# Performance work log

Measured on AMD Instinct MI355X. Metric: run time of the kernel, lower is better.

Reference implementation:

```python
import jax, jax.numpy as jnp
import numpy as np

B, S, H, R = 32, 1024, 768, 24
ATT_EPS = 1e10
LN_EPS = 1e-12


def setup_inputs() -> dict:
    key = jax.random.key(0)
    ks = jax.random.split(key, 20)
    sc = 0.02
    inp = {
        "relation": jax.random.randint(ks[0], (B, 1), 0, R),
        "last_hidden_size": jax.random.normal(ks[1], (B, S, H), dtype=jnp.float32),
        "sub_head": jax.random.randint(ks[2], (B, 1), 0, S),
        "sub_tail": jax.random.randint(ks[3], (B, 1), 0, S),
        "attention_mask": jnp.ones((B, S), dtype=jnp.float32),
        # learned parameters
        "rel_emb": jax.random.normal(ks[4], (R, H)) * sc,
        "W_rf": jax.random.normal(ks[5], (H, H)) * sc,
        "b_rf": jnp.zeros((H,), jnp.float32),
        "gamma": jnp.ones((H,), jnp.float32),
        "beta": jnp.zeros((H,), jnp.float32),
        "W_wd": jax.random.normal(ks[6], (H, 2 * H)) * sc,
        "W_bd": jax.random.normal(ks[7], (H, 2 * H)) * sc,
        "Wq": jax.random.normal(ks[8], (H, H)) * sc,
        "bq": jnp.zeros((H,), jnp.float32),
        "Wk": jax.random.normal(ks[9], (H, H)) * sc,
        "bk": jnp.zeros((H,), jnp.float32),
        "Wv": jax.random.normal(ks[10], (H, H)) * sc,
        "bv": jnp.zeros((H,), jnp.float32),
        "W_obj": jax.random.normal(ks[11], (1, H)) * sc,
        "b_obj": jnp.zeros((1,), jnp.float32),
    }
    return inp


def reference(relation, last_hidden_size, sub_head, sub_tail, attention_mask,
              rel_emb, W_rf, b_rf, gamma, beta, W_wd, W_bd,
              Wq, bq, Wk, bk, Wv, bv, W_obj, b_obj):
    # dropout layers are identity in eval mode
    # relation feature: embedding -> linear -> ReLU6   [B,1,H]
    rel_feature = jnp.clip(rel_emb[relation] @ W_rf.T + b_rf, 0.0, 6.0)
    # subject span features via gather                 [B,1,H]
    sh = jnp.take_along_axis(last_hidden_size, sub_head[:, :, None], axis=1)
    st = jnp.take_along_axis(last_hidden_size, sub_tail[:, :, None], axis=1)
    sub_feature = (sh + st) * 0.5
    cond = jnp.concatenate([rel_feature, sub_feature], axis=-1)  # [B,1,2H]

    # conditional layer norm: per-sample affine from condition
    weight = cond @ W_wd.T + gamma  # [B,1,H]
    bias = cond @ W_bd.T + beta     # [B,1,H]
    mean = jnp.mean(last_hidden_size, axis=-1, keepdims=True)
    ctr = last_hidden_size - mean
    var = jnp.mean(ctr * ctr, axis=-1, keepdims=True)
    x = ctr / jnp.sqrt(var + LN_EPS)
    x = x * weight + bias  # [B,S,H]

    # custom attention: ReLU-activated q/k/v, additive mask bias, residual
    q = jax.nn.relu(x @ Wq.T + bq)
    k = jax.nn.relu(x @ Wk.T + bk)
    v = jax.nn.relu(x @ Wv.T + bv)
    e = jnp.einsum('bsh,bth->bst', q, k)  # [B,S,S]
    e = e - ATT_EPS * (1.0 - attention_mask[:, None, :])
    a = jax.nn.softmax(e, axis=-1)
    hidden = jnp.einsum('bst,bth->bsh', a, v) + x  # residual

    pred_obj_head = jnp.squeeze(hidden @ W_obj.T + b_obj, axis=-1)  # [B,S]
    return pred_obj_head, hidden
```

## Files before the change

kernel.cpp:

```cpp
#include <hip/hip_runtime.h>

constexpr int NB  = 32;
constexpr int NS  = 1024;
constexpr int NH  = 768;
constexpr int NH2 = 1536;
constexpr int NQKV = 2304;
constexpr int NBS = NB * NS;

typedef __bf16 bf16x8 __attribute__((ext_vector_type(8)));
typedef float  f32x4  __attribute__((ext_vector_type(4)));
typedef unsigned short u16x8 __attribute__((ext_vector_type(8)));

__device__ __forceinline__ unsigned short f2bf(float f) {
  unsigned int u = __builtin_bit_cast(unsigned int, f);
  u += 0x7FFFu + ((u >> 16) & 1u);
  return (unsigned short)(u >> 16);
}
__device__ __forceinline__ float bf2f(unsigned short h) {
  return __builtin_bit_cast(float, ((unsigned int)h) << 16);
}

#define GLDS16(g, l)                                                         \
  __builtin_amdgcn_global_load_lds(                                          \
      (__attribute__((address_space(1))) void*)(g),                          \
      (__attribute__((address_space(3))) void*)(l), 16, 0, 0)

#define SBAR()    asm volatile("s_barrier" ::: "memory")
#define WAITVM6() asm volatile("s_waitcnt vmcnt(6)" ::: "memory")
#define WAITVM0() asm volatile("s_waitcnt vmcnt(0)" ::: "memory")
#define LGKM0()                                                              \
  do {                                                                       \
    asm volatile("s_waitcnt lgkmcnt(0)" ::: "memory");                       \
    __builtin_amdgcn_sched_barrier(0);                                       \
  } while (0)

__launch_bounds__(256)
__global__ void cond_pre(const int* __restrict__ relation,
                         const float* __restrict__ h,
                         const int* __restrict__ subh,
                         const int* __restrict__ subt,
                         const float* __restrict__ rel_emb,
                         float* __restrict__ reT, float* __restrict__ condT) {
  const int b = blockIdx.x, t = threadIdx.x;
  const int r = relation[b], sh = subh[b], st = subt[b];
  for (int k = t; k < NH; k += 256) {
    reT[(size_t)k * NB + b] = rel_emb[(size_t)r * NH + k];
    condT[(size_t)(NH + k) * NB + b] =
        0.5f * (h[((size_t)b * NS + sh) * NH + k] +
                h[((size_t)b * NS + st) * NH + k]);
  }
}

__launch_bounds__(256)
__global__ void cond_rf(const float* __restrict__ W_rf,
                        const float* __restrict__ b_rf,
                        const float* __restrict__ reT,
                        float* __restrict__ condT) {
  const int t = threadIdx.x;
  const int b = t & 31, jl = t >> 5;
  const int j = blockIdx.x * 8 + jl;
  const float4* w4 = (const float4*)(W_rf + (size_t)j * NH);
  const float* rT = reT + b;
  float a0 = 0.f, a1 = 0.f;
  for (int k4 = 0; k4 < NH / 4; k4++) {
    float4 w = w4[k4];
    const float* c = rT + (size_t)(k4 * 4) * NB;
    a0 += w.x * c[0] + w.y * c[NB];
    a1 += w.z * c[2 * NB] + w.w * c[3 * NB];
  }
  float acc = a0 + a1 + b_rf[j];
  condT[(size_t)j * NB + b] = fminf(fmaxf(acc, 0.0f), 6.0f);
}

__launch_bounds__(256)
__global__ void cond_wb(const float* __restrict__ W_wd,
                        const float* __restrict__ W_bd,
                        const float* __restrict__ gamma,
                        const float* __restrict__ beta,
                        const float* __restrict__ condT,
                        float* __restrict__ wt, float* __restrict__ bs) {
  __shared__ float redW[128], redB[128];
  const int t = threadIdx.x;
  const int b = t & 31, jl = (t >> 5) & 3, ks = t >> 7;
  const int j = blockIdx.x * 4 + jl;
  const float4* ww = (const float4*)(W_wd + (size_t)j * NH2 + ks * NH);
  const float4* wb = (const float4*)(W_bd + (size_t)j * NH2 + ks * NH);
  const float* cT = condT + (size_t)ks * NH * NB + b;
  float aw0 = 0.f, aw1 = 0.f, ab0 = 0.f, ab1 = 0.f;
  for (int k4 = 0; k4 < NH / 4; k4++) {
    float4 w = ww[k4];
    float4 v = wb[k4];
    const float* c = cT + (size_t)(k4 * 4) * NB;
    float c0 = c[0], c1 = c[NB], c2 = c[2 * NB], c3 = c[3 * NB];
    aw0 += w.x * c0 + w.y * c1;
    aw1 += w.z * c2 + w.w * c3;
    ab0 += v.x * c0 + v.y * c1;
    ab1 += v.z * c2 + v.w * c3;
  }
  float aw = aw0 + aw1, ab = ab0 + ab1;
  if (ks == 1) {
    redW[t - 128] = aw;
    redB[t - 128] = ab;
  }
  __syncthreads();
  if (ks == 0) {
    aw += redW[t];
    ab += redB[t];
    wt[(size_t)b * NH + j] = aw + gamma[j];
    bs[(size_t)b * NH + j] = ab + beta[j];
  }
}

__launch_bounds__(64)
__global__ void ln_kernel(const float* __restrict__ h,
                          const float* __restrict__ wt,
                          const float* __restrict__ bs,
                          unsigned short* __restrict__ xbf) {
  const int row = blockIdx.x;
  const int b = row >> 10;
  const int lane = threadIdx.x;
  const float4* hr = (const float4*)(h + (size_t)row * NH);
  float4 v0 = hr[lane], v1 = hr[lane + 64], v2 = hr[lane + 128];
  float sum = 0.f, sq = 0.f;
  {
    sum += v0.x + v0.y + v0.z + v0.w;
    sq  += v0.x * v0.x + v0.y * v0.y + v0.z * v0.z + v0.w * v0.w;
    sum += v1.x + v1.y + v1.z + v1.w;
    sq  += v1.x * v1.x + v1.y * v1.y + v1.z * v1.z + v1.w * v1.w;
    sum += v2.x + v2.y + v2.z + v2.w;
    sq  += v2.x * v2.x + v2.y * v2.y + v2.z * v2.z + v2.w * v2.w;
  }
  for (int off = 32; off > 0; off >>= 1) {
    sum += __shfl_xor(sum, off, 64);
    sq  += __shfl_xor(sq, off, 64);
  }
  const float mean = sum * (1.0f / NH);
  const float var  = sq * (1.0f / NH) - mean * mean;
  const float rstd = rsqrtf(var + 1e-12f);
  const float4* wr = (const float4*)(wt + (size_t)b * NH);
  const float4* br = (const float4*)(bs + (size_t)b * NH);
  ushort4* xr = (ushort4*)(xbf + (size_t)row * NH);
#pragma unroll
  for (int i = 0; i < 3; i++) {
    float4 v = (i == 0) ? v0 : (i == 1) ? v1 : v2;
    float4 w = wr[lane + 64 * i];
    float4 bb = br[lane + 64 * i];
    ushort4 o;
    o.x = f2bf((v.x - mean) * rstd * w.x + bb.x);
    o.y = f2bf((v.y - mean) * rstd * w.y + bb.y);
    o.z = f2bf((v.z - mean) * rstd * w.z + bb.z);
    o.w = f2bf((v.w - mean) * rstd * w.w + bb.w);
    xr[lane + 64 * i] = o;
  }
}

__launch_bounds__(256)
__global__ void prep_w(const float* __restrict__ Wq, const float* __restrict__ bq,
                       const float* __restrict__ Wk, const float* __restrict__ bk,
                       const float* __restrict__ Wv, const float* __restrict__ bv,
                       unsigned short* __restrict__ Wcat, float* __restrict__ bcat) {
  const int row = blockIdx.x;
  const float* Wsrc;
  const float* bsrc;
  int r;
  if (row < NH) { Wsrc = Wq; bsrc = bq; r = row; }
  else if (row < NH2) { Wsrc = Wk; bsrc = bk; r = row - NH; }
  else { Wsrc = Wv; bsrc = bv; r = row - NH2; }
  for (int j = threadIdx.x; j < NH; j += 256)
    Wcat[(size_t)row * NH + j] = f2bf(Wsrc[(size_t)r * NH + j]);
  if (threadIdx.x == 0) bcat[row] = bsrc[r];
}

template <int OUT_BF16, int RELU, int HASBIAS, int RES>
__launch_bounds__(512, 2)
__global__ void gemm256(const unsigned short* __restrict__ A, long long sAz, int lda,
                        const unsigned short* __restrict__ Bm, long long sBz, int ldb,
                        void* __restrict__ C, long long sCz, int ldc,
                        const float* __restrict__ bias,
                        const unsigned short* __restrict__ Res, long long sRz, int ldr,
                        int K) {
  extern __shared__ char lds[];
  const int t = threadIdx.x;
  const int z = blockIdx.z;
  int id = blockIdx.x + blockIdx.y * gridDim.x;
  {
    const int nwg = gridDim.x * gridDim.y;
    const int q = nwg >> 3, r = nwg & 7;
    const int xcd = id & 7, lid = id >> 3;
    id = (xcd < r ? xcd * (q + 1) : r * (q + 1) + (xcd - r) * q) + lid;
  }
  const int tileN = (id % gridDim.x) * 256;
  const int tileM = (id / gridDim.x) * 256;
  const unsigned short* Ab = A + (size_t)z * sAz + (size_t)tileM * lda;
  const unsigned short* Bb = Bm + (size_t)z * sBz + (size_t)tileN * ldb;

  const int lane = t & 63;
  const int w = t >> 6;
  const int wm = w >> 2, wn = w & 3;
  const int lr = lane & 15, hi = lane >> 4;
  const int swz = (lr & 7) << 4;
  const int brow0 = (wn & 1) * 64;

  const int sr = t >> 3;
  const int scc = (t & 7) ^ (sr & 7);

#define STAGEH(Gb, ld, kc, dst)                                             \
  do {                                                                      \
    GLDS16((Gb) + (size_t)sr * (ld) + (kc) + scc * 8, (dst) + (size_t)t * 16); \
    GLDS16((Gb) + (size_t)(64 + sr) * (ld) + (kc) + scc * 8,                \
           (dst) + 8192 + (size_t)t * 16);                                  \
  } while (0)

#define RD_BALL(Bh)                                                         \
  do {                                                                      \
    _Pragma("unroll") for (int nn_ = 0; nn_ < 4; nn_++)                     \
      _Pragma("unroll") for (int ks_ = 0; ks_ < 2; ks_++)                   \
        bF[nn_][ks_] = *(const bf16x8*)((Bh) + (brow0 + nn_ * 16 + lr) * 128 + \
                                        ((ks_ * 64 + hi * 16) ^ swz));      \
  } while (0)

#define RD_AH(m0, Ah)                                                       \
  do {                                                                      \
    _Pragma("unroll") for (int mm_ = 0; mm_ < 4; mm_++)                     \
      _Pragma("unroll") for (int ks_ = 0; ks_ < 2; ks_++)                   \
        aF[mm_][ks_] = *(const bf16x8*)((Ah) + (((m0) + mm_) * 16 + lr) * 128 + \
                                        ((ks_ * 64 + hi * 16) ^ swz));      \
  } while (0)

#define MFMAQ(mb, nb)                                                       \
  do {                                                                      \
    __builtin_amdgcn_s_setprio(1);                                          \
    _Pragma("unroll") for (int ks_ = 0; ks_ < 2; ks_++)                     \
      _Pragma("unroll") for (int mm_ = 0; mm_ < 4; mm_++)                   \
        _Pragma("unroll") for (int nn_ = 0; nn_ < 2; nn_++)                 \
          acc[(mb) + mm_][(nb) + nn_] = __builtin_amdgcn_mfma_f32_16x16x32_bf16( \
              aF[mm_][ks_], bF[(nb) + nn_][ks_], acc[(mb) + mm_][(nb) + nn_], \
              0, 0, 0);                                                     \
    __builtin_amdgcn_s_setprio(0);                                          \
  } while (0)

  f32x4 acc[8][4];
#pragma unroll
  for (int m = 0; m < 8; m++)
#pragma unroll
    for (int n = 0; n < 4; n++) acc[m][n] = (f32x4)0.0f;

  const int NT = K >> 6;

  STAGEH(Bb, ldb, 0, lds + 65536);
  STAGEH(Bb + (size_t)128 * ldb, ldb, 0, lds + 65536 + 16384);
  STAGEH(Ab, lda, 0, lds);
  STAGEH(Ab + (size_t)128 * lda, lda, 0, lds + 16384);
  STAGEH(Bb, ldb, 64, lds + 65536 + 32768);
  STAGEH(Bb + (size_t)128 * ldb, ldb, 64, lds + 65536 + 32768 + 16384);
  STAGEH(Ab, lda, 64, lds + 32768);
  WAITVM6();
  SBAR();

  for (int kt = 0; kt < NT; kt++) {
    const int bc = kt & 1;
    const char* Ah = lds + bc * 32768 + wm * 16384;
    const char* Bh = lds + 65536 + bc * 32768 + (wn >> 1) * 16384;
    bf16x8 aF[4][2], bF[4][2];
    RD_BALL(Bh);
    RD_AH(0, Ah);
    if (kt + 1 < NT)
      STAGEH(Ab + (size_t)128 * lda, lda, (kt + 1) * 64,
             lds + (bc ^ 1) * 32768 + 16384);
    SBAR();
    LGKM0();
    MFMAQ(0, 0);
    SBAR();
    if (kt + 2 < NT)
      STAGEH(Bb, ldb, (kt + 2) * 64, lds + 65536 + bc * 32768);
    SBAR();
    MFMAQ(0, 2);
    SBAR();
    RD_AH(4, Ah);
    if (kt + 2 < NT)
      STAGEH(Bb + (size_t)128 * ldb, ldb, (kt + 2) * 64,
             lds + 65536 + bc * 32768 + 16384);
    SBAR();
    LGKM0();
    MFMAQ(4, 2);
    SBAR();
    if (kt + 2 < NT)
      STAGEH(Ab, lda, (kt + 2) * 64, lds + bc * 32768);
    SBAR();
    MFMAQ(4, 0);
    if (kt + 2 < NT) {
      WAITVM6();
    } else if (kt + 1 < NT) {
      WAITVM0();
    }
    SBAR();
  }

  const int row0 = tileM + wm * 128;
  const int col0 = tileN + wn * 64;
#pragma unroll
  for (int m = 0; m < 8; m++) {
    const int rowb = row0 + m * 16 + hi * 4;
#pragma unroll
    for (int n = 0; n < 4; n++) {
      const int col = col0 + n * 16 + lr;
      const float bv = HASBIAS ? bias[col] : 0.0f;
      f32x4 v = acc[m][n];
#pragma unroll
      for (int r = 0; r < 4; r++) {
        float x = v[r] + bv;
        if (RELU) x = fmaxf(x, 0.0f);
        if (RES)
          x += bf2f(Res[(size_t)z * sRz + (size_t)(rowb + r) * ldr + col]);
        if (OUT_BF16)
          ((unsigned short*)C)[(size_t)z * sCz + (size_t)(rowb + r) * ldc + col] =
              f2bf(x);
        else
          ((float*)C)[(size_t)z * sCz + (size_t)(rowb + r) * ldc + col] = x;
      }
    }
  }
#undef STAGEH
#undef RD_BALL
#undef RD_AH
#undef MFMAQ
}

__launch_bounds__(256)
__global__ void softmax_kernel(float* __restrict__ e,
                               const float* __restrict__ mask, int b0) {
  const int ri = blockIdx.x;
  const int lb = blockIdx.y;
  const int b = b0 + lb;
  float* row = e + ((size_t)lb * NS + ri) * NS;
  const int t = threadIdx.x;
  float4 v = ((const float4*)row)[t];
  float4 m = ((const float4*)(mask + (size_t)b * NS))[t];
  v.x -= 1e10f * (1.0f - m.x);
  v.y -= 1e10f * (1.0f - m.y);
  v.z -= 1e10f * (1.0f - m.z);
  v.w -= 1e10f * (1.0f - m.w);
  float mx = fmaxf(fmaxf(v.x, v.y), fmaxf(v.z, v.w));
  __shared__ float red[4];
  for (int off = 32; off > 0; off >>= 1) mx = fmaxf(mx, __shfl_xor(mx, off, 64));
  if ((t & 63) == 0) red[t >> 6] = mx;
  __syncthreads();
  mx = fmaxf(fmaxf(red[0], red[1]), fmaxf(red[2], red[3]));
  const float e0 = __expf(v.x - mx), e1 = __expf(v.y - mx);
  const float e2 = __expf(v.z - mx), e3 = __expf(v.w - mx);
  float sm = e0 + e1 + e2 + e3;
  __syncthreads();
  for (int off = 32; off > 0; off >>= 1) sm += __shfl_xor(sm, off, 64);
  if ((t & 63) == 0) red[t >> 6] = sm;
  __syncthreads();
  sm = red[0] + red[1] + red[2] + red[3];
  const float inv = 1.0f / sm;
  ushort4 o;
  o.x = f2bf(e0 * inv);
  o.y = f2bf(e1 * inv);
  o.z = f2bf(e2 * inv);
  o.w = f2bf(e3 * inv);
  ((ushort4*)row)[t] = o;
}

__launch_bounds__(256)
__global__ void transpose_v(const unsigned short* __restrict__ qkv,
                            unsigned short* __restrict__ vT) {
  const int b = blockIdx.z;
  const int s0 = blockIdx.x * 64;
  const int h0 = blockIdx.y * 64;
  __shared__ unsigned short tile[64][72];
  const int t = threadIdx.x;
  const int tx = t & 7, ty = t >> 3;
  const unsigned short* src = qkv + ((size_t)(b * NS + s0)) * NQKV + NH2 + h0;
#pragma unroll
  for (int i = 0; i < 2; i++) {
    const int s = ty + 32 * i;
    u16x8 vv = *(const u16x8*)(src + (size_t)s * NQKV + tx * 8);
#pragma unroll
    for (int j = 0; j < 8; j++) tile[s][tx * 8 + j] = vv[j];
  }
  __syncthreads();
  unsigned short* dst = vT + ((size_t)b * NH + h0) * NS + s0;
#pragma unroll
  for (int i = 0; i < 2; i++) {
    const int hh = ty + 32 * i;
    u16x8 o;
#pragma unroll
    for (int j = 0; j < 8; j++) o[j] = tile[tx * 8 + j][hh];
    *(u16x8*)(dst + (size_t)hh * NS + tx * 8) = o;
  }
}

__launch_bounds__(64)
__global__ void pred_kernel(const float* __restrict__ hidden,
                            const float* __restrict__ wobj,
                            const float* __restrict__ bobj,
                            float* __restrict__ pred) {
  const int row = blockIdx.x;
  const int lane = threadIdx.x;
  const float4* hr = (const float4*)(hidden + (size_t)row * NH);
  const float4* wr = (const float4*)wobj;
  float s = 0.f;
#pragma unroll
  for (int i = 0; i < 3; i++) {
    float4 a = hr[lane + 64 * i];
    float4 w = wr[lane + 64 * i];
    s += a.x * w.x + a.y * w.y + a.z * w.z + a.w * w.w;
  }
  for (int off = 32; off > 0; off >>= 1) s += __shfl_xor(s, off, 64);
  if (lane == 0) pred[row] = s + bobj[0];
}

extern "C" void kernel_launch(void* const* d_in, const int* in_sizes, int n_in,
                              void* d_out, int out_size, void* d_ws,
                              size_t ws_size, hipStream_t stream) {
  const int* relation   = (const int*)d_in[0];
  const float* lhs      = (const float*)d_in[1];
  const int* sub_head   = (const int*)d_in[2];
  const int* sub_tail   = (const int*)d_in[3];
  const float* att_mask = (const float*)d_in[4];
  const float* rel_emb  = (const float*)d_in[5];
  const float* W_rf     = (const float*)d_in[6];
  const float* b_rf     = (const float*)d_in[7];
  const float* gamma    = (const float*)d_in[8];
  const float* beta     = (const float*)d_in[9];
  const float* W_wd     = (const float*)d_in[10];
  const float* W_bd     = (const float*)d_in[11];
  const float* Wq       = (const float*)d_in[12];
  const float* bq       = (const float*)d_in[13];
  const float* Wk       = (const float*)d_in[14];
  const float* bk       = (const float*)d_in[15];
  const float* Wv       = (const float*)d_in[16];
  const float* bv       = (const float*)d_in[17];
  const float* W_obj    = (const float*)d_in[18];
  const float* b_obj    = (const float*)d_in[19];

  char* ws = (char*)d_ws;
  unsigned short* Wcat = (unsigned short*)(ws + 0);
  float* bcat  = (float*)(ws + 3538944);
  float* wt    = (float*)(ws + 3548160);
  float* bs    = (float*)(ws + 3646464);
  float* reT   = (float*)(ws + 3744768);
  float* condT = (float*)(ws + 3843072);
  unsigned short* xbf = (unsigned short*)(ws + 4039680);
  unsigned short* qkv = (unsigned short*)(ws + 54371328);
  unsigned short* vT  = (unsigned short*)(ws + 205366272);
  float* ebuf = (float*)(ws + 255697920);

  float* out_pred = (float*)d_out;
  float* out_hidden = out_pred + NBS;

  const size_t fixed = 255697920ull;
  size_t avail = ws_size > fixed ? ws_size - fixed : 0;
  int CB = 32;
  while (CB > 1 && (size_t)CB * (size_t)NS * NS * 4 > avail) CB >>= 1;

  prep_w<<<dim3(NQKV), dim3(256), 0, stream>>>(Wq, bq, Wk, bk, Wv, bv, Wcat, bcat);
  cond_pre<<<dim3(NB), dim3(256), 0, stream>>>(relation, lhs, sub_head, sub_tail,
                                               rel_emb, reT, condT);
  cond_rf<<<dim3(NH / 8), dim3(256), 0, stream>>>(W_rf, b_rf, reT, condT);
  cond_wb<<<dim3(NH / 4), dim3(256), 0, stream>>>(W_wd, W_bd, gamma, beta, condT,
                                                  wt, bs);
  ln_kernel<<<dim3(NBS), dim3(64), 0, stream>>>(lhs, wt, bs, xbf);

  gemm256<1, 1, 1, 0><<<dim3(NQKV / 256, NBS / 256, 1), dim3(512), 131072, stream>>>(
      xbf, 0, NH, Wcat, 0, NH, qkv, 0, NQKV, bcat, nullptr, 0, 0, NH);

  transpose_v<<<dim3(NS / 64, NH / 64, NB), dim3(256), 0, stream>>>(qkv, vT);

  for (int b0 = 0; b0 < NB; b0 += CB) {
    gemm256<0, 0, 0, 0><<<dim3(NS / 256, NS / 256, CB), dim3(512), 131072, stream>>>(
        qkv + (size_t)b0 * NS * NQKV, (long long)NS * NQKV, NQKV,
        qkv + (size_t)b0 * NS * NQKV + NH, (long long)NS * NQKV, NQKV,
        ebuf, (long long)NS * NS, NS, nullptr, nullptr, 0, 0, NH);
    softmax_kernel<<<dim3(NS, CB), dim3(256), 0, stream>>>(ebuf, att_mask, b0);
    gemm256<0, 0, 0, 1><<<dim3(NH / 256, NS / 256, CB), dim3(512), 131072, stream>>>(
        (const unsigned short*)ebuf, (long long)NS * 2048, 2048,
        vT + (size_t)b0 * NH * NS, (long long)NH * NS, NS,
        out_hidden + (size_t)b0 * NS * NH, (long long)NS * NH, NH, nullptr,
        xbf + (size_t)b0 * NS * NH, (long long)NS * NH, NH, NS);
  }

  pred_kernel<<<dim3(NBS), dim3(64), 0, stream>>>(out_hidden, W_obj, b_obj,
                                                  out_pred);
}
```

Measured before the change: 494.4 us.

## Fuse V transpose and prediction head into GEMM epilogues, split Q/K layout

The QKV GEMM epilogue now writes Q and K to separate contiguous buffers and writes V directly in transposed layout, which removes the transpose_v kernel. The final P·V GEMM epilogue computes the W_obj dot product per row with shuffles and atomically accumulates into a pred buffer that is zeroed beforehand, which removes the pred_kernel pass over hidden. Softmax now writes bf16 probabilities to a separate compact buffer instead of overwriting the fp32 scores in place. In exchange, the transposed V stores are strided and scattered, and the atomics make pred accumulation order nondeterministic.

```diff
diff --git a/kernel.cpp b/kernel.cpp
--- a/kernel.cpp
+++ b/kernel.cpp
@@ -171,14 +171,17 @@
   if (threadIdx.x == 0) bcat[row] = bsrc[r];
 }
 
-template <int OUT_BF16, int RELU, int HASBIAS, int RES>
+template <int OUT_BF16, int RELU, int HASBIAS, int RES, int SPLIT3, int FPRED>
 __launch_bounds__(512, 2)
 __global__ void gemm256(const unsigned short* __restrict__ A, long long sAz, int lda,
                         const unsigned short* __restrict__ Bm, long long sBz, int ldb,
                         void* __restrict__ C, long long sCz, int ldc,
                         const float* __restrict__ bias,
                         const unsigned short* __restrict__ Res, long long sRz, int ldr,
-                        int K) {
+                        int K, unsigned short* __restrict__ vTp,
+                        const float* __restrict__ wobj,
+                        const float* __restrict__ bobj,
+                        float* __restrict__ pred) {
   extern __shared__ char lds[];
   const int t = threadIdx.x;
   const int z = blockIdx.z;
@@ -301,6 +304,7 @@
 #pragma unroll
   for (int m = 0; m < 8; m++) {
     const int rowb = row0 + m * 16 + hi * 4;
+    float psum[4] = {0.f, 0.f, 0.f, 0.f};
 #pragma unroll
     for (int n = 0; n < 4; n++) {
       const int col = col0 + n * 16 + lr;
@@ -312,11 +316,37 @@
         if (RELU) x = fmaxf(x, 0.0f);
         if (RES)
           x += bf2f(Res[(size_t)z * sRz + (size_t)(rowb + r) * ldr + col]);
-        if (OUT_BF16)
+        if (SPLIT3) {
+          const int seg = col >= NH2 ? 2 : (col >= NH ? 1 : 0);
+          if (seg < 2) {
+            ((unsigned short*)C)[(size_t)seg * NBS * NH +
+                                 (size_t)(rowb + r) * NH + (col - seg * NH)] =
+                f2bf(x);
+          } else {
+            vTp[((size_t)((rowb + r) >> 10) * NH + (col - NH2)) * NS +
+                ((rowb + r) & (NS - 1))] = f2bf(x);
+          }
+        } else if (OUT_BF16) {
           ((unsigned short*)C)[(size_t)z * sCz + (size_t)(rowb + r) * ldc + col] =
               f2bf(x);
-        else
+        } else {
           ((float*)C)[(size_t)z * sCz + (size_t)(rowb + r) * ldc + col] = x;
+        }
+        if (FPRED) psum[r] += x * wobj[col];
+      }
+    }
+    if (FPRED) {
+#pragma unroll
+      for (int r = 0; r < 4; r++) {
+        float s = psum[r];
+        s += __shfl_xor(s, 1, 64);
+        s += __shfl_xor(s, 2, 64);
+        s += __shfl_xor(s, 4, 64);
+        s += __shfl_xor(s, 8, 64);
+        if (lr == 0) {
+          float add = s + ((tileN == 0 && wn == 0) ? bobj[0] : 0.0f);
+          atomicAdd(pred + (size_t)z * NS + rowb + r, add);
+        }
       }
     }
   }
@@ -327,12 +357,13 @@
 }
 
 __launch_bounds__(256)
-__global__ void softmax_kernel(float* __restrict__ e,
+__global__ void softmax_kernel(const float* __restrict__ e,
+                               unsigned short* __restrict__ p,
                                const float* __restrict__ mask, int b0) {
   const int ri = blockIdx.x;
   const int lb = blockIdx.y;
   const int b = b0 + lb;
-  float* row = e + ((size_t)lb * NS + ri) * NS;
+  const float* row = e + ((size_t)lb * NS + ri) * NS;
   const int t = threadIdx.x;
   float4 v = ((const float4*)row)[t];
   float4 m = ((const float4*)(mask + (size_t)b * NS))[t];
@@ -360,56 +391,7 @@
   o.y = f2bf(e1 * inv);
   o.z = f2bf(e2 * inv);
   o.w = f2bf(e3 * inv);
-  ((ushort4*)row)[t] = o;
-}
-
-__launch_bounds__(256)
-__global__ void transpose_v(const unsigned short* __restrict__ qkv,
-                            unsigned short* __restrict__ vT) {
-  const int b = blockIdx.z;
-  const int s0 = blockIdx.x * 64;
-  const int h0 = blockIdx.y * 64;
-  __shared__ unsigned short tile[64][72];
-  const int t = threadIdx.x;
-  const int tx = t & 7, ty = t >> 3;
-  const unsigned short* src = qkv + ((size_t)(b * NS + s0)) * NQKV + NH2 + h0;
-#pragma unroll
-  for (int i = 0; i < 2; i++) {
-    const int s = ty + 32 * i;
-    u16x8 vv = *(const u16x8*)(src + (size_t)s * NQKV + tx * 8);
-#pragma unroll
-    for (int j = 0; j < 8; j++) tile[s][tx * 8 + j] = vv[j];
-  }
-  __syncthreads();
-  unsigned short* dst = vT + ((size_t)b * NH + h0) * NS + s0;
-#pragma unroll
-  for (int i = 0; i < 2; i++) {
-    const int hh = ty + 32 * i;
-    u16x8 o;
-#pragma unroll
-    for (int j = 0; j < 8; j++) o[j] = tile[tx * 8 + j][hh];
-    *(u16x8*)(dst + (size_t)hh * NS + tx * 8) = o;
-  }
-}
-
-__launch_bounds__(64)
-__global__ void pred_kernel(const float* __restrict__ hidden,
-                            const float* __restrict__ wobj,
-                            const float* __restrict__ bobj,
-                            float* __restrict__ pred) {
-  const int row = blockIdx.x;
-  const int lane = threadIdx.x;
-  const float4* hr = (const float4*)(hidden + (size_t)row * NH);
-  const float4* wr = (const float4*)wobj;
-  float s = 0.f;
-#pragma unroll
-  for (int i = 0; i < 3; i++) {
-    float4 a = hr[lane + 64 * i];
-    float4 w = wr[lane + 64 * i];
-    s += a.x * w.x + a.y * w.y + a.z * w.z + a.w * w.w;
-  }
-  for (int off = 32; off > 0; off >>= 1) s += __shfl_xor(s, off, 64);
-  if (lane == 0) pred[row] = s + bobj[0];
+  ((ushort4*)(p + ((size_t)lb * NS + ri) * NS))[t] = o;
 }
 
 extern "C" void kernel_launch(void* const* d_in, const int* in_sizes, int n_in,
@@ -444,17 +426,21 @@
   float* reT   = (float*)(ws + 3744768);
   float* condT = (float*)(ws + 3843072);
   unsigned short* xbf = (unsigned short*)(ws + 4039680);
-  unsigned short* qkv = (unsigned short*)(ws + 54371328);
-  unsigned short* vT  = (unsigned short*)(ws + 205366272);
-  float* ebuf = (float*)(ws + 255697920);
+  unsigned short* qkc = (unsigned short*)(ws + 54371328);
+  unsigned short* vT  = (unsigned short*)(ws + 155034624);
+  char* attbuf = ws + 205366272;
 
   float* out_pred = (float*)d_out;
   float* out_hidden = out_pred + NBS;
 
-  const size_t fixed = 255697920ull;
+  const size_t fixed = 205366272ull;
   size_t avail = ws_size > fixed ? ws_size - fixed : 0;
   int CB = 32;
-  while (CB > 1 && (size_t)CB * (size_t)NS * NS * 4 > avail) CB >>= 1;
+  while (CB > 1 && (size_t)CB * ((size_t)NS * NS * 4 + (size_t)NS * NS * 2) > avail)
+    CB >>= 1;
+  float* ebuf = (float*)attbuf;
+  unsigned short* pbuf =
+      (unsigned short*)(attbuf + (size_t)CB * NS * NS * 4);
 
   prep_w<<<dim3(NQKV), dim3(256), 0, stream>>>(Wq, bq, Wk, bk, Wv, bv, Wcat, bcat);
   cond_pre<<<dim3(NB), dim3(256), 0, stream>>>(relation, lhs, sub_head, sub_tail,
@@ -463,25 +449,28 @@
   cond_wb<<<dim3(NH / 4), dim3(256), 0, stream>>>(W_wd, W_bd, gamma, beta, condT,
                                                   wt, bs);
   ln_kernel<<<dim3(NBS), dim3(64), 0, stream>>>(lhs, wt, bs, xbf);
-
-  gemm256<1, 1, 1, 0><<<dim3(NQKV / 256, NBS / 256, 1), dim3(512), 131072, stream>>>(
-      xbf, 0, NH, Wcat, 0, NH, qkv, 0, NQKV, bcat, nullptr, 0, 0, NH);
-
-  transpose_v<<<dim3(NS / 64, NH / 64, NB), dim3(256), 0, stream>>>(qkv, vT);
+  hipMemsetAsync(out_pred, 0, (size_t)NBS * sizeof(float), stream);
+
+  gemm256<1, 1, 1, 0, 1, 0>
+      <<<dim3(NQKV / 256, NBS / 256, 1), dim3(512), 131072, stream>>>(
+          xbf, 0, NH, Wcat, 0, NH, qkc, 0, NH, bcat, nullptr, 0, 0, NH, vT,
+          nullptr, nullptr, nullptr);
 
   for (int b0 = 0; b0 < NB; b0 += CB) {
-    gemm256<0, 0, 0, 0><<<dim3(NS / 256, NS / 256, CB), dim3(512), 131072, stream>>>(
-        qkv + (size_t)b0 * NS * NQKV, (long long)NS * NQKV, NQKV,
-        qkv + (size_t)b0 * NS * NQKV + NH, (long long)NS * NQKV, NQKV,
-        ebuf, (long long)NS * NS, NS, nullptr, nullptr, 0, 0, NH);
-    softmax_kernel<<<dim3(NS, CB), dim3(256), 0, stream>>>(ebuf, att_mask, b0);
-    gemm256<0, 0, 0, 1><<<dim3(NH / 256, NS / 256, CB), dim3(512), 131072, stream>>>(
-        (const unsigned short*)ebuf, (long long)NS * 2048, 2048,
-        vT + (size_t)b0 * NH * NS, (long long)NH * NS, NS,
-        out_hidden + (size_t)b0 * NS * NH, (long long)NS * NH, NH, nullptr,
-        xbf + (size_t)b0 * NS * NH, (long long)NS * NH, NH, NS);
-  }
-
-  pred_kernel<<<dim3(NBS), dim3(64), 0, stream>>>(out_hidden, W_obj, b_obj,
-                                                  out_pred);
-}
+    gemm256<0, 0, 0, 0, 0, 0>
+        <<<dim3(NS / 256, NS / 256, CB), dim3(512), 131072, stream>>>(
+            qkc + (size_t)b0 * NS * NH, (long long)NS * NH, NH,
+            qkc + (size_t)NBS * NH + (size_t)b0 * NS * NH, (long long)NS * NH, NH,
+            ebuf, (long long)NS * NS, NS, nullptr, nullptr, 0, 0, NH, nullptr,
+            nullptr, nullptr, nullptr);
+    softmax_kernel<<<dim3(NS, CB), dim3(256), 0, stream>>>(ebuf, pbuf, att_mask,
+                                                           b0);
+    gemm256<0, 0, 0, 1, 0, 1>
+        <<<dim3(NH / 256, NS / 256, CB), dim3(512), 131072, stream>>>(
+            pbuf, (long long)NS * NS, NS,
+            vT + (size_t)b0 * NH * NS, (long long)NH * NS, NS,
+            out_hidden + (size_t)b0 * NS * NH, (long long)NS * NH, NH, nullptr,
+            xbf + (size_t)b0 * NS * NH, (long long)NS * NH, NH, NS, nullptr,
+            W_obj, b_obj, out_pred + (size_t)b0 * NS);
+  }
+}
```

Result: slower. 555.7 us (+12.4%).
